# Kernel tuning notes

Measured on AMD Instinct MI355X. Metric: run time of the kernel, lower is better.

The kernel has to match this reference:

```python
import jax, jax.numpy as jnp
import numpy as np
from jax import lax


def _grey_opening_2d(x, size):
    """scipy.ndimage.grey_opening(x, size) per 2D map, applied over trailing (H, W).

    Grey opening = erosion (min filter) then dilation (max filter) with a
    size x size flat structuring element. scipy uses mode='reflect'
    (== np.pad 'symmetric') and, for even sizes, an asymmetric window:
    erosion covers offsets [-(size//2), size - size//2 - 1], dilation uses
    the mirrored offsets. x: [B, C, H, W].
    """
    lo = size // 2
    hi = size - size // 2 - 1
    window = (1, 1, size, size)
    ones = (1, 1, 1, 1)

    # Erosion: min filter, window offsets [-lo, hi]
    xe = jnp.pad(x, ((0, 0), (0, 0), (lo, hi), (lo, hi)), mode='symmetric')
    er = lax.reduce_window(xe, jnp.inf, lax.min, window, ones, 'VALID')

    # Dilation: max filter with mirrored structuring element -> offsets [-hi, lo]
    xd = jnp.pad(er, ((0, 0), (0, 0), (hi, lo), (hi, lo)), mode='symmetric')
    di = lax.reduce_window(xd, -jnp.inf, lax.max, window, ones, 'VALID')
    return di


def setup_inputs() -> dict:
    key = jax.random.key(0)
    labels = jax.random.uniform(key, (16, 8, 512, 512), dtype=jnp.float32)
    return {"labels": labels}


def reference(labels):
    radius = 2
    smooth = _grey_opening_2d(labels, radius)
    smooth = lax.stop_gradient(smooth)  # original detaches the opened target
    return jnp.mean((labels - smooth) ** 2)
```

## Files before the change

### kernel.cpp

```cpp
#include <hip/hip_runtime.h>


constexpr int W = 512;
constexpr int H = 512;
constexpr int RPW = 16;
constexpr int STRIPS_PER_IMG = H / RPW;

__device__ __forceinline__ void load_row8(const float* p, float v[8]) {
  float4 a = *reinterpret_cast<const float4*>(p);
  float4 b = *reinterpret_cast<const float4*>(p + 4);
  v[0] = a.x; v[1] = a.y; v[2] = a.z; v[3] = a.w;
  v[4] = b.x; v[5] = b.y; v[6] = b.z; v[7] = b.w;
}

__device__ __forceinline__ void colmin8(const float v[8], float cm[8], int lane) {
  float left = __shfl_up(v[7], 1);
  if (lane == 0) left = v[0];
  cm[0] = fminf(left, v[0]);
#pragma unroll
  for (int k = 1; k < 8; ++k) cm[k] = fminf(v[k - 1], v[k]);
}

__device__ __forceinline__ void colmax8(const float e[8], float dm[8], int lane) {
  float right = __shfl_down(e[0], 1);
  if (lane == 63) right = e[7];
#pragma unroll
  for (int k = 0; k < 7; ++k) dm[k] = fmaxf(e[k], e[k + 1]);
  dm[7] = fmaxf(e[7], right);
}

__global__ __launch_bounds__(256) void open_loss_partial(
    const float* __restrict__ x, float* __restrict__ partial, int nWaves) {
  const int tid = blockIdx.x * blockDim.x + threadIdx.x;
  const int wave = tid >> 6;
  const int lane = threadIdx.x & 63;

  float acc = 0.f;
  if (wave < nWaves) {
    const int img = wave / STRIPS_PER_IMG;
    const int strip = wave % STRIPS_PER_IMG;
    const float* base = x + (size_t)img * (H * W) + lane * 8;
    const int rs = strip * RPW;
    const int re = rs + RPW - 1;

    float xp[8], cmp[8], dmp[8];
    float v[8], cm[8], er[8];

    load_row8(base + (size_t)(rs > 0 ? rs - 1 : 0) * W, v);
    colmin8(v, cmp, lane);

    load_row8(base + (size_t)rs * W, v);
    colmin8(v, cm, lane);
#pragma unroll
    for (int k = 0; k < 8; ++k) er[k] = fminf(cmp[k], cm[k]);
    colmax8(er, dmp, lane);
#pragma unroll
    for (int k = 0; k < 8; ++k) { xp[k] = v[k]; cmp[k] = cm[k]; }

    for (int i = rs; i <= re; ++i) {
      if (i < H - 1) {
        load_row8(base + (size_t)(i + 1) * W, v);
        colmin8(v, cm, lane);
        float dmn[8];
#pragma unroll
        for (int k = 0; k < 8; ++k) er[k] = fminf(cmp[k], cm[k]);
        colmax8(er, dmn, lane);
#pragma unroll
        for (int k = 0; k < 8; ++k) {
          float di = fmaxf(dmp[k], dmn[k]);
          float d = xp[k] - di;
          acc = fmaf(d, d, acc);
          xp[k] = v[k]; cmp[k] = cm[k]; dmp[k] = dmn[k];
        }
      } else {
#pragma unroll
        for (int k = 0; k < 8; ++k) {
          float d = xp[k] - dmp[k];
          acc = fmaf(d, d, acc);
        }
      }
    }
  }

#pragma unroll
  for (int off = 32; off > 0; off >>= 1) acc += __shfl_down(acc, off);
  __shared__ float sh[4];
  const int wid = threadIdx.x >> 6;
  if (lane == 0) sh[wid] = acc;
  __syncthreads();
  if (threadIdx.x == 0) partial[blockIdx.x] = sh[0] + sh[1] + sh[2] + sh[3];
}

__global__ __launch_bounds__(256) void reduce_final(
    const float* __restrict__ partial, int n, float* __restrict__ out,
    double invN) {
  double s = 0.0;
  for (int i = threadIdx.x; i < n; i += blockDim.x) s += (double)partial[i];
#pragma unroll
  for (int off = 32; off > 0; off >>= 1) s += __shfl_down(s, off);
  __shared__ double sh[4];
  const int wid = threadIdx.x >> 6;
  if ((threadIdx.x & 63) == 0) sh[wid] = s;
  __syncthreads();
  if (threadIdx.x == 0) {
    double tot = sh[0] + sh[1] + sh[2] + sh[3];
    out[0] = (float)(tot * invN);
  }
}

extern "C" void kernel_launch(void* const* d_in, const int* in_sizes, int n_in,
                              void* d_out, int out_size, void* d_ws, size_t ws_size,
                              hipStream_t stream) {
  const float* x = (const float*)d_in[0];
  float* out = (float*)d_out;
  float* partial = (float*)d_ws;

  const long long n = in_sizes[0];
  const int nImg = (int)(n / ((long long)H * W));
  const int nWaves = nImg * STRIPS_PER_IMG;
  const int nBlocks = nWaves / 4;

  open_loss_partial<<<nBlocks, 256, 0, stream>>>(x, partial, nWaves);
  reduce_final<<<1, 256, 0, stream>>>(partial, nBlocks, out,
                                      1.0 / (double)n);
}
```

Measured before the change: 189.0 us.

## Fuse final reduction via atomicAdd and replace shuffles with neighbor loads

Removes the second reduction kernel by having each block atomically add its scaled partial sum into the output, after a memset. Horizontal neighbor values now come from extra scalar global loads instead of cross-lane shuffles. This also lets the row loop run as a fixed-count, partially unrolled loop with no per-row boundary branch. The trade-off is float atomics, which make the summation order nondeterministic and lose some precision compared with the double-precision final reduce, plus extra scalar loads per row.

```diff
diff --git a/kernel.cpp b/kernel.cpp
--- a/kernel.cpp
+++ b/kernel.cpp
@@ -4,81 +4,88 @@
 constexpr int W = 512;
 constexpr int H = 512;
 constexpr int RPW = 16;
-constexpr int STRIPS_PER_IMG = H / RPW;
+constexpr int STRIPS = H / RPW;
 
-__device__ __forceinline__ void load_row8(const float* p, float v[8]) {
-  float4 a = *reinterpret_cast<const float4*>(p);
-  float4 b = *reinterpret_cast<const float4*>(p + 4);
-  v[0] = a.x; v[1] = a.y; v[2] = a.z; v[3] = a.w;
-  v[4] = b.x; v[5] = b.y; v[6] = b.z; v[7] = b.w;
-}
+__global__ __launch_bounds__(256) void open_loss(
+    const float* __restrict__ x, float* __restrict__ out, float invN) {
+  const int gtid = blockIdx.x * blockDim.x + threadIdx.x;
+  const int wave = gtid >> 6;
+  const int lane = threadIdx.x & 63;
+  const int img = wave >> 5;
+  const int strip = wave & (STRIPS - 1);
 
-__device__ __forceinline__ void colmin8(const float v[8], float cm[8], int lane) {
-  float left = __shfl_up(v[7], 1);
-  if (lane == 0) left = v[0];
-  cm[0] = fminf(left, v[0]);
+  const float* base =
+      x + ((size_t)img * H + (size_t)strip * RPW) * W + (size_t)lane * 8;
+
+  float v[8], cm[8], cm8;
+  float pcm[8], pcm8;
+  float xp[8], dmp[8];
+  const int loff = (lane == 0) ? 0 : -1;
+  const int roff = (lane == 63) ? 7 : 8;
+
+  auto loadrow = [&](int drow) {
+    const float* p = base + (ptrdiff_t)drow * W;
+    float4 a = *reinterpret_cast<const float4*>(p);
+    float4 b = *reinterpret_cast<const float4*>(p + 4);
+    v[0] = a.x; v[1] = a.y; v[2] = a.z; v[3] = a.w;
+    v[4] = b.x; v[5] = b.y; v[6] = b.z; v[7] = b.w;
+    const float left = p[loff];
+    const float right = p[roff];
+    cm[0] = fminf(left, v[0]);
 #pragma unroll
-  for (int k = 1; k < 8; ++k) cm[k] = fminf(v[k - 1], v[k]);
-}
+    for (int k = 1; k < 8; ++k) cm[k] = fminf(v[k - 1], v[k]);
+    cm8 = fminf(v[7], right);
+  };
 
-__device__ __forceinline__ void colmax8(const float e[8], float dm[8], int lane) {
-  float right = __shfl_down(e[0], 1);
-  if (lane == 63) right = e[7];
+  loadrow(strip ? -1 : 0);
 #pragma unroll
-  for (int k = 0; k < 7; ++k) dm[k] = fmaxf(e[k], e[k + 1]);
-  dm[7] = fmaxf(e[7], right);
-}
+  for (int k = 0; k < 8; ++k) pcm[k] = cm[k];
+  pcm8 = cm8;
 
-__global__ __launch_bounds__(256) void open_loss_partial(
-    const float* __restrict__ x, float* __restrict__ partial, int nWaves) {
-  const int tid = blockIdx.x * blockDim.x + threadIdx.x;
-  const int wave = tid >> 6;
-  const int lane = threadIdx.x & 63;
+  loadrow(0);
+  {
+    float er[8];
+#pragma unroll
+    for (int k = 0; k < 8; ++k) er[k] = fminf(pcm[k], cm[k]);
+    const float er8 = fminf(pcm8, cm8);
+#pragma unroll
+    for (int k = 0; k < 7; ++k) dmp[k] = fmaxf(er[k], er[k + 1]);
+    dmp[7] = fmaxf(er[7], er8);
+#pragma unroll
+    for (int k = 0; k < 8; ++k) { xp[k] = v[k]; pcm[k] = cm[k]; }
+    pcm8 = cm8;
+  }
 
   float acc = 0.f;
-  if (wave < nWaves) {
-    const int img = wave / STRIPS_PER_IMG;
-    const int strip = wave % STRIPS_PER_IMG;
-    const float* base = x + (size_t)img * (H * W) + lane * 8;
-    const int rs = strip * RPW;
-    const int re = rs + RPW - 1;
 
-    float xp[8], cmp[8], dmp[8];
-    float v[8], cm[8], er[8];
+  auto advance = [&](int drow_next) {
+    loadrow(drow_next);
+    float er[8], dmn[8];
+#pragma unroll
+    for (int k = 0; k < 8; ++k) er[k] = fminf(pcm[k], cm[k]);
+    const float er8 = fminf(pcm8, cm8);
+#pragma unroll
+    for (int k = 0; k < 7; ++k) dmn[k] = fmaxf(er[k], er[k + 1]);
+    dmn[7] = fmaxf(er[7], er8);
+#pragma unroll
+    for (int k = 0; k < 8; ++k) {
+      const float d = xp[k] - fmaxf(dmp[k], dmn[k]);
+      acc = fmaf(d, d, acc);
+      xp[k] = v[k]; pcm[k] = cm[k]; dmp[k] = dmn[k];
+    }
+    pcm8 = cm8;
+  };
 
-    load_row8(base + (size_t)(rs > 0 ? rs - 1 : 0) * W, v);
-    colmin8(v, cmp, lane);
+#pragma unroll 5
+  for (int r = 1; r <= RPW - 1; ++r) advance(r);
 
-    load_row8(base + (size_t)rs * W, v);
-    colmin8(v, cm, lane);
+  if (strip != STRIPS - 1) {
+    advance(RPW);
+  } else {
 #pragma unroll
-    for (int k = 0; k < 8; ++k) er[k] = fminf(cmp[k], cm[k]);
-    colmax8(er, dmp, lane);
-#pragma unroll
-    for (int k = 0; k < 8; ++k) { xp[k] = v[k]; cmp[k] = cm[k]; }
-
-    for (int i = rs; i <= re; ++i) {
-      if (i < H - 1) {
-        load_row8(base + (size_t)(i + 1) * W, v);
-        colmin8(v, cm, lane);
-        float dmn[8];
-#pragma unroll
-        for (int k = 0; k < 8; ++k) er[k] = fminf(cmp[k], cm[k]);
-        colmax8(er, dmn, lane);
-#pragma unroll
-        for (int k = 0; k < 8; ++k) {
-          float di = fmaxf(dmp[k], dmn[k]);
-          float d = xp[k] - di;
-          acc = fmaf(d, d, acc);
-          xp[k] = v[k]; cmp[k] = cm[k]; dmp[k] = dmn[k];
-        }
-      } else {
-#pragma unroll
-        for (int k = 0; k < 8; ++k) {
-          float d = xp[k] - dmp[k];
-          acc = fmaf(d, d, acc);
-        }
-      }
+    for (int k = 0; k < 8; ++k) {
+      const float d = xp[k] - dmp[k];
+      acc = fmaf(d, d, acc);
     }
   }
 
@@ -88,23 +95,8 @@
   const int wid = threadIdx.x >> 6;
   if (lane == 0) sh[wid] = acc;
   __syncthreads();
-  if (threadIdx.x == 0) partial[blockIdx.x] = sh[0] + sh[1] + sh[2] + sh[3];
-}
-
-__global__ __launch_bounds__(256) void reduce_final(
-    const float* __restrict__ partial, int n, float* __restrict__ out,
-    double invN) {
-  double s = 0.0;
-  for (int i = threadIdx.x; i < n; i += blockDim.x) s += (double)partial[i];
-#pragma unroll
-  for (int off = 32; off > 0; off >>= 1) s += __shfl_down(s, off);
-  __shared__ double sh[4];
-  const int wid = threadIdx.x >> 6;
-  if ((threadIdx.x & 63) == 0) sh[wid] = s;
-  __syncthreads();
   if (threadIdx.x == 0) {
-    double tot = sh[0] + sh[1] + sh[2] + sh[3];
-    out[0] = (float)(tot * invN);
+    atomicAdd(out, (sh[0] + sh[1] + sh[2] + sh[3]) * invN);
   }
 }
 
@@ -113,14 +105,14 @@
                               hipStream_t stream) {
   const float* x = (const float*)d_in[0];
   float* out = (float*)d_out;
-  float* partial = (float*)d_ws;
 
   const long long n = in_sizes[0];
   const int nImg = (int)(n / ((long long)H * W));
-  const int nWaves = nImg * STRIPS_PER_IMG;
+  const int nWaves = nImg * STRIPS;
   const int nBlocks = nWaves / 4;
 
-  open_loss_partial<<<nBlocks, 256, 0, stream>>>(x, partial, nWaves);
-  reduce_final<<<1, 256, 0, stream>>>(partial, nBlocks, out,
-                                      1.0 / (double)n);
+  const float invN = 1.0f / (float)n;
+
+  hipMemsetAsync(out, 0, sizeof(float), stream);
+  open_loss<<<nBlocks, 256, 0, stream>>>(x, out, invN);
 }
```

Result: slower. 193.8 us (+2.5%).
